# Kernel optimization log

Measured on AMD Instinct MI355X. Metric: run time of the kernel, lower is better.

## Reference

```python
import jax, jax.numpy as jnp
import numpy as np
from jax import lax

B, T, F, C = 2, 249, 64, 256   # fixed by alpha/beta weight shapes in build()
K = 3                          # conv kernel size
FILT = 256                     # q/k conv filters (both blocks)
V = 256                        # v conv filters (both blocks)
OUT_CH = 64                    # conv2d_final filters (hardcoded)


def conv2d(x, w, b):
    # NHWC 'same' conv, stride 1, dilation 1
    return lax.conv_general_dilated(
        x, w, window_strides=(1, 1), padding='SAME',
        dimension_numbers=('NHWC', 'HWIO', 'NHWC')) + b


def attn_block(x, wq, bq, wk, bk, wv, bv):
    # x: [B, H, L, C]; attention over L per (batch, H) slice
    q = conv2d(x, wq, bq)          # [B,H,L,FILT]
    k = conv2d(x, wk, bk)          # [B,H,L,FILT]
    v = conv2d(x, wv, bv)          # [B,H,L,V]
    scores = jnp.einsum('bhqc,bhkc->bhqk', q, k)   # [B,H,L,L]
    dist = jax.nn.softmax(scores, axis=-1)
    return jnp.einsum('bhqk,bhkc->bhqc', dist, v)  # [B,H,L,V]


def setup_inputs() -> dict:
    key = jax.random.key(0)
    ks = jax.random.split(key, 18)
    s = 0.05
    d = {'x': jax.random.normal(ks[0], (B, T, F, C), jnp.float32)}
    names = ['wq_f', 'wk_f', 'wv_f', 'wq_t', 'wk_t', 'wv_t']
    outs = [FILT, FILT, V, FILT, FILT, V]
    for i, (n, o) in enumerate(zip(names, outs)):
        d[n] = jax.random.normal(ks[1 + i], (K, K, C, o), jnp.float32) * s
        d['b' + n[1:]] = jnp.zeros((o,), jnp.float32)
    d['w_final'] = jax.random.normal(ks[8], (K, K, V + V + C, OUT_CH), jnp.float32) * s
    d['b_final'] = jnp.zeros((OUT_CH,), jnp.float32)
    d['alpha'] = jax.random.uniform(ks[9], (B, T, F, V), jnp.float32, -0.05, 0.05)
    d['beta'] = jax.random.uniform(ks[10], (B, T, F, V), jnp.float32, -0.05, 0.05)
    return d


def reference(x, wq_f, bq_f, wk_f, bk_f, wv_f, bv_f,
              wq_t, bq_t, wk_t, bk_t, wv_t, bv_t,
              w_final, b_final, alpha, beta):
    # AFAB: transpose to [B,F,T,C], attend over time axis T
    xt = jnp.transpose(x, (0, 2, 1, 3))
    out_freq = attn_block(xt, wq_f, bq_f, wk_f, bk_f, wv_f, bv_f)
    out_freq = jnp.transpose(out_freq, (0, 2, 1, 3))  # back to [B,T,F,V]
    # ATAB: attend over frequency axis F directly on [B,T,F,C]
    out_time = attn_block(x, wq_t, bq_t, wk_t, bk_t, wv_t, bv_t)
    # learned elementwise gating + concat + final conv (concatenation=True path)
    fused = jnp.concatenate([alpha * out_freq, beta * out_time, x], axis=-1)
    return conv2d(fused, w_final, b_final)
```

## Files before the change

### kernel.cpp

```cpp
#include <hip/hip_runtime.h>


typedef _Float16 f16;
typedef _Float16 f16x8 __attribute__((ext_vector_type(8)));
typedef float    f32x4 __attribute__((ext_vector_type(4)));

#define B_   2
#define T_   249
#define F_   64
#define TP   251
#define FP   66
#define PIXB (T_*F_)
#define NPIX (B_*PIXB)
#define LPAD 256
#define XPOS (B_*TP*FP)

static constexpr size_t FUSED_BYTES = (size_t)B_*TP*FP*768*2;
static constexpr size_t XPAD_BYTES  = (size_t)B_*TP*FP*256*2;
static constexpr size_t QF_BYTES    = (size_t)B_*64*LPAD*256*2;
static constexpr size_t QT_BYTES    = (size_t)B_*T_*64*256*2;
static constexpr size_t WT_BYTES    = (size_t)9*1536*256*2;
static constexpr size_t WFT_BYTES   = (size_t)9*64*768*2;

static constexpr size_t OFF_FUSED = 0;
static constexpr size_t OFF_XPAD  = OFF_FUSED + FUSED_BYTES;
static constexpr size_t OFF_QF    = OFF_XPAD  + XPAD_BYTES;
static constexpr size_t OFF_KF    = OFF_QF + QF_BYTES;
static constexpr size_t OFF_VF    = OFF_KF + QF_BYTES;
static constexpr size_t OFF_QT    = OFF_VF + QF_BYTES;
static constexpr size_t OFF_KT    = OFF_QT + QT_BYTES;
static constexpr size_t OFF_VT    = OFF_KT + QT_BYTES;
static constexpr size_t OFF_WT    = OFF_VT + QT_BYTES;
static constexpr size_t OFF_WFT   = OFF_WT + WT_BYTES;
static constexpr size_t OFF_BALL  = OFF_WFT + WFT_BYTES;
static constexpr size_t OFF_BF    = OFF_BALL + 1536*4;
static constexpr size_t WS_NEED   = OFF_BF + 64*4;

__device__ __forceinline__ f32x4 mfma16(f16x8 a, f16x8 b, f32x4 c) {
    return __builtin_amdgcn_mfma_f32_16x16x32_f16(a, b, c, 0, 0, 0);
}

__device__ __forceinline__ void gl_lds16(const void* g, void* l) {
    __builtin_amdgcn_global_load_lds(
        (const __attribute__((address_space(1))) unsigned int*)(unsigned long long)g,
        (__attribute__((address_space(3))) unsigned int*)(unsigned int)(unsigned long long)l,
        16, 0, 0);
}

__global__ __launch_bounds__(256) void prep_w(
    const float* __restrict__ wqf, const float* __restrict__ wkf, const float* __restrict__ wvf,
    const float* __restrict__ wqt, const float* __restrict__ wkt, const float* __restrict__ wvt,
    const float* __restrict__ wfin,
    const float* __restrict__ bqf, const float* __restrict__ bkf, const float* __restrict__ bvf,
    const float* __restrict__ bqt, const float* __restrict__ bkt, const float* __restrict__ bvt,
    const float* __restrict__ bfin,
    f16* __restrict__ wT, f16* __restrict__ wfT,
    float* __restrict__ biasAll, float* __restrict__ biasF)
{
    int idx = blockIdx.x*256 + threadIdx.x;
    if (idx < 9*1536*256) {
        int tap = idx / (1536*256);
        int r   = idx - tap*(1536*256);
        int n = r >> 8, c = r & 255;
        int dt = tap/3 - 1, df = tap%3 - 1;
        int blk = n >> 8, nl = n & 255;
        const float* w; int kh, kw;
        if (blk < 3) { w = (blk==0) ? wqf : (blk==1) ? wkf : wvf; kh = df+1; kw = dt+1; }
        else         { w = (blk==3) ? wqt : (blk==4) ? wkt : wvt; kh = dt+1; kw = df+1; }
        wT[idx] = (f16)w[((kh*3 + kw)*256 + c)*256 + nl];
    }
    if (idx < 9*64*768) {
        int tap = idx / (64*768);
        int r   = idx - tap*(64*768);
        int oc = r / 768, cin = r - oc*768;
        int dt = tap/3 - 1, df = tap%3 - 1;
        wfT[idx] = (f16)wfin[(((dt+1)*3 + (df+1))*768 + cin)*64 + oc];
    }
    if (idx < 1536) {
        int blk = idx >> 8, nl = idx & 255;
        const float* bb = (blk==0)?bqf:(blk==1)?bkf:(blk==2)?bvf:(blk==3)?bqt:(blk==4)?bkt:bvt;
        biasAll[idx] = bb[nl];
    }
    if (idx < 64) biasF[idx] = bfin[idx];
}

__global__ __launch_bounds__(256) void prep_x(
    const float* __restrict__ x, f16* __restrict__ xpad, f16* __restrict__ fused)
{
    int tid = blockIdx.x*256 + threadIdx.x;
    int pix = tid >> 5, c8 = (tid & 31)*8;
    int b = pix / PIXB; int r = pix - b*PIXB;
    int t = r >> 6, f = r & 63;
    const float* src = x + (size_t)pix*256 + c8;
    f16x8 v;
#pragma unroll
    for (int j = 0; j < 8; ++j) v[j] = (f16)src[j];
    size_t pp = (size_t)(b*TP + t + 1)*FP + (f + 1);
    *(f16x8*)(xpad + pp*256 + c8) = v;
    *(f16x8*)(fused + pp*768 + 512 + c8) = v;
}

__global__ __launch_bounds__(256) void border_zero(
    f16* __restrict__ xpad, f16* __restrict__ fused)
{
    int pix = blockIdx.x*2 + (threadIdx.x >> 7);
    int tl = threadIdx.x & 127;
    int b = pix / 630; int i = pix - b*630;
    int tp, fp;
    if (i < 66)       { tp = 0;   fp = i; }
    else if (i < 132) { tp = 250; fp = i - 66; }
    else { int j = i - 132; tp = 1 + (j >> 1); fp = (j & 1) * 65; }
    size_t pp = (size_t)(b*TP + tp)*FP + fp;
    f16x8 z = {0, 0, 0, 0, 0, 0, 0, 0};
    if (tl < 32) *(f16x8*)(xpad + pp*256 + tl*8) = z;
    if (tl < 96) *(f16x8*)(fused + pp*768 + tl*8) = z;
}

__global__ __launch_bounds__(512, 2) void conv_qkv(
    const f16* __restrict__ xpad, const f16* __restrict__ wT,
    const float* __restrict__ biasAll,
    f16* __restrict__ qf, f16* __restrict__ kf, f16* __restrict__ vf,
    f16* __restrict__ qt, f16* __restrict__ kt_, f16* __restrict__ vt)
{
    __shared__ f16 smemH[448*64];
    __shared__ f16 smemB[2][256*64];

    const int xcd = blockIdx.x & 7, lin = blockIdx.x >> 3;
    const int mtcnt = (xcd < 6) ? 16 : 15;
    if (lin >= 6*mtcnt) return;
    const int mtbase = (xcd < 6) ? xcd*16 : 96 + (xcd - 6)*15;
    const int nt = lin / mtcnt;
    const int mt = mtbase + (lin - nt*mtcnt);

    const int bb_ = mt / 63;
    const int t0  = (mt - bb_*63) * 4;
    const int Gs66 = (bb_*TP + t0) * 66;

    const int l   = threadIdx.x & 63;
    const int wid = threadIdx.x >> 6;
    const int wm = wid >> 2, wn = wid & 3;

    int hOff[7];
#pragma unroll
    for (int j = 0; j < 7; ++j) {
        int pos = j*64 + wid*8 + (l >> 3);
        int ps = pos;
        if (ps > 395) ps = 395;
        { int pm = XPOS - 1 - (bb_*TP + t0)*66; if (ps > pm) ps = pm; }
        int ch = (l & 7) ^ (ps & 7);
        hOff[j] = (Gs66 + ps)*256 + ch*8;
    }
    int bSrc[4];
#pragma unroll
    for (int j = 0; j < 4; ++j) {
        int row = j*64 + wid*8 + (l >> 3);
        int ch = (l & 7) ^ (row & 7);
        bSrc[j] = (nt*256 + row)*256 + ch*8;
    }

    int pos00[8];
#pragma unroll
    for (int m = 0; m < 8; ++m) {
        int r = wm*128 + m*16 + (l & 15);
        pos00[m] = ((r >> 6) + 1)*66 + (r & 63) + 1;
    }
    int bRow[4], bSw[4];
#pragma unroll
    for (int n = 0; n < 4; ++n) {
        int row = wn*64 + n*16 + (l & 15);
        bRow[n] = row*64; bSw[n] = row & 7;
    }

    f32x4 acc[8][4];
#pragma unroll
    for (int m = 0; m < 8; ++m)
#pragma unroll
        for (int n = 0; n < 4; ++n) acc[m][n] = {0.f, 0.f, 0.f, 0.f};

#define HSTAGE(C) do {                                                         \
        _Pragma("unroll")                                                      \
        for (int j_ = 0; j_ < 7; ++j_)                                         \
            gl_lds16(xpad + hOff[j_] + (C)*64,                                 \
                     smemH + (j_*512 + wid*64)*8);                             \
    } while (0)

#define BSTAGE(TAP, C, NB) do {                                                \
        const f16* wt_ = wT + (size_t)(TAP)*(1536*256) + (C)*64;               \
        _Pragma("unroll")                                                      \
        for (int j_ = 0; j_ < 4; ++j_)                                         \
            gl_lds16(wt_ + bSrc[j_], &smemB[NB][(j_*512 + wid*64)*8]);         \
    } while (0)

#define QCOMP(NB, TAPOFF) do {                                                 \
        int pos_[8];                                                           \
        _Pragma("unroll")                                                      \
        for (int m = 0; m < 8; ++m) pos_[m] = pos00[m] + (TAPOFF);             \
        _Pragma("unroll")                                                      \
        for (int kk = 0; kk < 2; ++kk) {                                       \
            const int cch = kk*4 + (l >> 4);                                   \
            f16x8 af[8], bf[4];                                                \
            _Pragma("unroll")                                                  \
            for (int m = 0; m < 8; ++m)                                        \
                af[m] = *(const f16x8*)(smemH + pos_[m]*64 + ((cch ^ (pos_[m] & 7)) << 3)); \
            _Pragma("unroll")                                                  \
            for (int n = 0; n < 4; ++n)                                        \
                bf[n] = *(const f16x8*)(&smemB[NB][0] + bRow[n] + ((cch ^ bSw[n]) << 3)); \
            __builtin_amdgcn_s_setprio(1);                                     \
            _Pragma("unroll")                                                  \
            for (int m = 0; m < 8; ++m)                                        \
                _Pragma("unroll")                                              \
                for (int n = 0; n < 4; ++n)                                    \
                    acc[m][n] = mfma16(af[m], bf[n], acc[m][n]);               \
            __builtin_amdgcn_s_setprio(0);                                     \
        }                                                                      \
    } while (0)

    int buf = 0;
    HSTAGE(0);
    BSTAGE(0, 0, 0);
    __syncthreads();
    for (int c = 0; c < 4; ++c) {
        for (int tap = 0; tap < 9; ++tap) {
            if (tap < 8)      BSTAGE(tap + 1, c, buf ^ 1);
            else if (c < 3)   BSTAGE(0, c + 1, buf ^ 1);
            const int dt = tap/3 - 1, df = tap - (tap/3)*3 - 1;
            QCOMP(buf, dt*66 + df);
            __syncthreads();
            buf ^= 1;
        }
        if (c < 3) {
            HSTAGE(c + 1);
            __syncthreads();
        }
    }
#undef HSTAGE
#undef BSTAGE
#undef QCOMP

    f16* dst = (nt==0)?qf:(nt==1)?kf:(nt==2)?vf:(nt==3)?qt:(nt==4)?kt_:vt;
#pragma unroll
    for (int m = 0; m < 8; ++m) {
#pragma unroll
        for (int rg = 0; rg < 4; ++rg) {
            int row = wm*128 + m*16 + (l >> 4)*4 + rg;
            int t = t0 + (row >> 6), f = row & 63;
            if (t <= 248) {
#pragma unroll
                for (int n = 0; n < 4; ++n) {
                    int col = wn*64 + n*16 + (l & 15);
                    float v = acc[m][n][rg] + biasAll[nt*256 + col];
                    int off;
                    if (nt < 2)       off = ((bb_*64 + f)*LPAD + t)*256 + col;
                    else if (nt == 2) off = ((bb_*64 + f)*256 + col)*LPAD + t;
                    else if (nt < 5)  off = ((bb_*T_ + t)*64 + f)*256 + col;
                    else              off = ((bb_*T_ + t)*256 + col)*64 + f;
                    dst[off] = (f16)v;
                }
            }
        }
    }
}

__global__ __launch_bounds__(256) void attn_f(
    const f16* __restrict__ qf, const f16* __restrict__ kf, const f16* __restrict__ vf,
    const float* __restrict__ alpha, f16* __restrict__ fused)
{
    __shared__ f16 plds[4][16*256];
    const int l = threadIdx.x & 63;
    const int wid = threadIdx.x >> 6;
    const int head = blockIdx.x >> 2;
    const int qb = blockIdx.x & 3;
    const int b = head >> 6, f = head & 63;
    const f16* qh = qf + (size_t)head*LPAD*256;
    const f16* kh = kf + (size_t)head*LPAD*256;
    const f16* vh = vf + (size_t)head*256*LPAD;
    const int qr0 = qb*64 + wid*16;
    f16* pw = &plds[wid][0];

    f16x8 qa[8];
#pragma unroll
    for (int ks = 0; ks < 8; ++ks)
        qa[ks] = *(const f16x8*)(qh + (qr0 + (l & 15))*256 + ks*32 + (l >> 4)*8);

    f32x4 s[16];
#pragma unroll
    for (int nf = 0; nf < 16; ++nf) s[nf] = {0.f, 0.f, 0.f, 0.f};
#pragma unroll
    for (int ks = 0; ks < 8; ++ks)
#pragma unroll
        for (int nf = 0; nf < 16; ++nf) {
            f16x8 bf = *(const f16x8*)(kh + (nf*16 + (l & 15))*256 + ks*32 + (l >> 4)*8);
            s[nf] = mfma16(qa[ks], bf, s[nf]);
        }

    float inv[4];
#pragma unroll
    for (int rg = 0; rg < 4; ++rg) {
        float m = -1e30f;
#pragma unroll
        for (int nf = 0; nf < 16; ++nf)
            if (nf*16 + (l & 15) < T_) m = fmaxf(m, s[nf][rg]);
#pragma unroll
        for (int d = 1; d < 16; d <<= 1) m = fmaxf(m, __shfl_xor(m, d, 64));
        float sum = 0.f;
#pragma unroll
        for (int nf = 0; nf < 16; ++nf) {
            float p = (nf*16 + (l & 15) < T_) ? __expf(s[nf][rg] - m) : 0.f;
            s[nf][rg] = p;
            sum += p;
        }
#pragma unroll
        for (int d = 1; d < 16; d <<= 1) sum += __shfl_xor(sum, d, 64);
        inv[rg] = 1.f / sum;
    }

#pragma unroll
    for (int nf = 0; nf < 16; ++nf)
#pragma unroll
        for (int rg = 0; rg < 4; ++rg) {
            int row = (l >> 4)*4 + rg;
            int col = nf*16 + (l & 15);
            int byte = (row*512 + col*2) ^ ((row & 7) << 4);
            *(f16*)((char*)pw + byte) = (f16)s[nf][rg];
        }

    f32x4 o[16];
#pragma unroll
    for (int nf = 0; nf < 16; ++nf) o[nf] = {0.f, 0.f, 0.f, 0.f};
#pragma unroll
    for (int ks = 0; ks < 8; ++ks) {
        int row = l & 15;
        int cch = ks*4 + (l >> 4);
        int byte = row*512 + ((cch ^ (row & 7)) << 4);
        f16x8 pa = *(const f16x8*)((const char*)pw + byte);
#pragma unroll
        for (int nf = 0; nf < 16; ++nf) {
            f16x8 bf = *(const f16x8*)(vh + (nf*16 + (l & 15))*LPAD + ks*32 + (l >> 4)*8);
            o[nf] = mfma16(pa, bf, o[nf]);
        }
    }

#pragma unroll
    for (int rg = 0; rg < 4; ++rg) {
        int t = qr0 + (l >> 4)*4 + rg;
        if (t < T_) {
#pragma unroll
            for (int nf = 0; nf < 16; ++nf) {
                int c = nf*16 + (l & 15);
                float v = o[nf][rg] * inv[rg] * alpha[((size_t)(b*T_ + t)*64 + f)*256 + c];
                fused[((size_t)(b*TP + t + 1)*FP + (f + 1))*768 + c] = (f16)v;
            }
        }
    }
}

__global__ __launch_bounds__(256) void attn_t(
    const f16* __restrict__ qt, const f16* __restrict__ kt, const f16* __restrict__ vt,
    const float* __restrict__ beta, f16* __restrict__ fused)
{
    __shared__ f16 plds[4][16*64];
    const int l = threadIdx.x & 63;
    const int wid = threadIdx.x >> 6;
    const int head = blockIdx.x;
    const int b = head / T_, t = head - b*T_;
    const f16* qh = qt + (size_t)head*64*256;
    const f16* kh = kt + (size_t)head*64*256;
    const f16* vh = vt + (size_t)head*256*64;
    const int qr0 = wid*16;
    f16* pw = &plds[wid][0];

    f16x8 qa[8];
#pragma unroll
    for (int ks = 0; ks < 8; ++ks)
        qa[ks] = *(const f16x8*)(qh + (qr0 + (l & 15))*256 + ks*32 + (l >> 4)*8);

    f32x4 s[4];
#pragma unroll
    for (int nf = 0; nf < 4; ++nf) s[nf] = {0.f, 0.f, 0.f, 0.f};
#pragma unroll
    for (int ks = 0; ks < 8; ++ks)
#pragma unroll
        for (int nf = 0; nf < 4; ++nf) {
            f16x8 bf = *(const f16x8*)(kh + (nf*16 + (l & 15))*256 + ks*32 + (l >> 4)*8);
            s[nf] = mfma16(qa[ks], bf, s[nf]);
        }

    float inv[4];
#pragma unroll
    for (int rg = 0; rg < 4; ++rg) {
        float m = -1e30f;
#pragma unroll
        for (int nf = 0; nf < 4; ++nf) m = fmaxf(m, s[nf][rg]);
#pragma unroll
        for (int d = 1; d < 16; d <<= 1) m = fmaxf(m, __shfl_xor(m, d, 64));
        float sum = 0.f;
#pragma unroll
        for (int nf = 0; nf < 4; ++nf) {
            float p = __expf(s[nf][rg] - m);
            s[nf][rg] = p;
            sum += p;
        }
#pragma unroll
        for (int d = 1; d < 16; d <<= 1) sum += __shfl_xor(sum, d, 64);
        inv[rg] = 1.f / sum;
    }

#pragma unroll
    for (int nf = 0; nf < 4; ++nf)
#pragma unroll
        for (int rg = 0; rg < 4; ++rg) {
            int row = (l >> 4)*4 + rg;
            int col = nf*16 + (l & 15);
            int byte = (row*128 + col*2) ^ ((row & 7) << 4);
            *(f16*)((char*)pw + byte) = (f16)s[nf][rg];
        }

    f32x4 o[16];
#pragma unroll
    for (int nf = 0; nf < 16; ++nf) o[nf] = {0.f, 0.f, 0.f, 0.f};
#pragma unroll
    for (int ks = 0; ks < 2; ++ks) {
        int row = l & 15;
        int cch = ks*4 + (l >> 4);
        int byte = row*128 + ((cch ^ (row & 7)) << 4);
        f16x8 pa = *(const f16x8*)((const char*)pw + byte);
#pragma unroll
        for (int nf = 0; nf < 16; ++nf) {
            f16x8 bf = *(const f16x8*)(vh + (nf*16 + (l & 15))*64 + ks*32 + (l >> 4)*8);
            o[nf] = mfma16(pa, bf, o[nf]);
        }
    }

#pragma unroll
    for (int rg = 0; rg < 4; ++rg) {
        int fo = qr0 + (l >> 4)*4 + rg;
#pragma unroll
        for (int nf = 0; nf < 16; ++nf) {
            int c = nf*16 + (l & 15);
            float v = o[nf][rg] * inv[rg] * beta[((size_t)(b*T_ + t)*64 + fo)*256 + c];
            fused[((size_t)(b*TP + t + 1)*FP + (fo + 1))*768 + 256 + c] = (f16)v;
        }
    }
}

__global__ __launch_bounds__(256, 2) void conv_final(
    const f16* __restrict__ fused, const f16* __restrict__ wfT,
    const float* __restrict__ biasF, float* __restrict__ out)
{
    __shared__ f16 smemH[288*64];
    __shared__ f16 smemB[2][64*64];

    const int mt = blockIdx.x;
    const int bb = mt / 125;
    const int t0 = (mt - bb*125) * 2;
    const int Gs66 = (bb*TP + t0) * 66;

    const int tid = threadIdx.x;
    const int l   = tid & 63;
    const int wid = tid >> 6;
    const int wm = wid >> 1, wn = wid & 1;

    int hOff[9];
#pragma unroll
    for (int j = 0; j < 9; ++j) {
        int ps = j*32 + (tid >> 3);
        if (ps > 263) ps = 263;
        { int pm = XPOS - 1 - (bb*TP + t0)*66; if (ps > pm) ps = pm; }
        int ch = (tid & 7) ^ (ps & 7);
        hOff[j] = (Gs66 + ps)*768 + ch*8;
    }
    int bSrc[2];
#pragma unroll
    for (int j = 0; j < 2; ++j) {
        int row = j*32 + (tid >> 3);
        int ch  = (tid & 7) ^ (row & 7);
        bSrc[j] = row*768 + ch*8;
    }

    int pos00[4];
#pragma unroll
    for (int m = 0; m < 4; ++m) {
        int r = wm*64 + m*16 + (l & 15);
        pos00[m] = ((r >> 6) + 1)*66 + (r & 63) + 1;
    }
    int bRow[2], bSw[2];
#pragma unroll
    for (int n = 0; n < 2; ++n) {
        int row = wn*32 + n*16 + (l & 15);
        bRow[n] = row*64; bSw[n] = row & 7;
    }

    f32x4 acc[4][2];
#pragma unroll
    for (int m = 0; m < 4; ++m)
#pragma unroll
        for (int n = 0; n < 2; ++n) acc[m][n] = {0.f, 0.f, 0.f, 0.f};

#define FHSTAGE(C) do {                                                        \
        _Pragma("unroll")                                                      \
        for (int j_ = 0; j_ < 9; ++j_)                                         \
            gl_lds16(fused + hOff[j_] + (C)*64,                                \
                     smemH + (j_*256 + wid*64)*8);                             \
    } while (0)

#define FBSTAGE(TAP, C, NB) do {                                               \
        const f16* wt_ = wfT + (size_t)(TAP)*(64*768) + (C)*64;                \
        _Pragma("unroll")                                                      \
        for (int j_ = 0; j_ < 2; ++j_)                                         \
            gl_lds16(wt_ + bSrc[j_], &smemB[NB][(j_*256 + wid*64)*8]);         \
    } while (0)

#define FCOMP(NB, TAPOFF) do {                                                 \
        int pos_[4];                                                           \
        _Pragma("unroll")                                                      \
        for (int m = 0; m < 4; ++m) pos_[m] = pos00[m] + (TAPOFF);             \
        _Pragma("unroll")                                                      \
        for (int kk = 0; kk < 2; ++kk) {                                       \
            const int cch = kk*4 + (l >> 4);                                   \
            f16x8 af[4], bf[2];                                                \
            _Pragma("unroll")                                                  \
            for (int m = 0; m < 4; ++m)                                        \
                af[m] = *(const f16x8*)(smemH + pos_[m]*64 + ((cch ^ (pos_[m] & 7)) << 3)); \
            _Pragma("unroll")                                                  \
            for (int n = 0; n < 2; ++n)                                        \
                bf[n] = *(const f16x8*)(&smemB[NB][0] + bRow[n] + ((cch ^ bSw[n]) << 3)); \
            __builtin_amdgcn_s_setprio(1);                                     \
            _Pragma("unroll")                                                  \
            for (int m = 0; m < 4; ++m)                                        \
                _Pragma("unroll")                                              \
                for (int n = 0; n < 2; ++n)                                    \
                    acc[m][n] = mfma16(af[m], bf[n], acc[m][n]);               \
            __builtin_amdgcn_s_setprio(0);                                     \
        }                                                                      \
    } while (0)

    int buf = 0;
    FHSTAGE(0);
    FBSTAGE(0, 0, 0);
    __syncthreads();
    for (int c = 0; c < 12; ++c) {
        for (int tap = 0; tap < 9; ++tap) {
            if (tap < 8)       FBSTAGE(tap + 1, c, buf ^ 1);
            else if (c < 11)   FBSTAGE(0, c + 1, buf ^ 1);
            const int dt = tap/3 - 1, df = tap - (tap/3)*3 - 1;
            FCOMP(buf, dt*66 + df);
            __syncthreads();
            buf ^= 1;
        }
        if (c < 11) {
            FHSTAGE(c + 1);
            __syncthreads();
        }
    }
#undef FHSTAGE
#undef FBSTAGE
#undef FCOMP

#pragma unroll
    for (int m = 0; m < 4; ++m) {
#pragma unroll
        for (int rg = 0; rg < 4; ++rg) {
            int r = wm*64 + m*16 + (l >> 4)*4 + rg;
            int t = t0 + (r >> 6), f = r & 63;
            if (t <= 248) {
                size_t pix = (size_t)bb*PIXB + t*64 + f;
#pragma unroll
                for (int n = 0; n < 2; ++n) {
                    int oc = wn*32 + n*16 + (l & 15);
                    out[pix*64 + oc] = acc[m][n][rg] + biasF[oc];
                }
            }
        }
    }
}

extern "C" void kernel_launch(void* const* d_in, const int* in_sizes, int n_in,
                              void* d_out, int out_size, void* d_ws, size_t ws_size,
                              hipStream_t stream) {
    (void)in_sizes; (void)n_in; (void)out_size;
    const float* x    = (const float*)d_in[0];
    const float* wqf  = (const float*)d_in[1];
    const float* bqf  = (const float*)d_in[2];
    const float* wkf  = (const float*)d_in[3];
    const float* bkf  = (const float*)d_in[4];
    const float* wvf  = (const float*)d_in[5];
    const float* bvf  = (const float*)d_in[6];
    const float* wqt  = (const float*)d_in[7];
    const float* bqt  = (const float*)d_in[8];
    const float* wkt  = (const float*)d_in[9];
    const float* bkt  = (const float*)d_in[10];
    const float* wvt  = (const float*)d_in[11];
    const float* bvt  = (const float*)d_in[12];
    const float* wfin = (const float*)d_in[13];
    const float* bfin = (const float*)d_in[14];
    const float* alpha= (const float*)d_in[15];
    const float* beta = (const float*)d_in[16];

    if (ws_size < WS_NEED) return;

    char* ws = (char*)d_ws;
    f16* fused  = (f16*)(ws + OFF_FUSED);
    f16* xpad   = (f16*)(ws + OFF_XPAD);
    f16* qf     = (f16*)(ws + OFF_QF);
    f16* kf     = (f16*)(ws + OFF_KF);
    f16* vf     = (f16*)(ws + OFF_VF);
    f16* qt     = (f16*)(ws + OFF_QT);
    f16* kt     = (f16*)(ws + OFF_KT);
    f16* vt     = (f16*)(ws + OFF_VT);
    f16* wT     = (f16*)(ws + OFF_WT);
    f16* wfT    = (f16*)(ws + OFF_WFT);
    float* bAll = (float*)(ws + OFF_BALL);
    float* bF   = (float*)(ws + OFF_BF);

    hipMemsetAsync(vf, 0, QF_BYTES, stream);

    border_zero<<<dim3(630), dim3(256), 0, stream>>>(xpad, fused);
    prep_w<<<dim3((9*1536*256 + 255)/256), dim3(256), 0, stream>>>(
        wqf, wkf, wvf, wqt, wkt, wvt, wfin,
        bqf, bkf, bvf, bqt, bkt, bvt, bfin, wT, wfT, bAll, bF);
    prep_x<<<dim3(NPIX*32/256), dim3(256), 0, stream>>>(x, xpad, fused);
    conv_qkv<<<dim3(768), dim3(512), 0, stream>>>(xpad, wT, bAll, qf, kf, vf, qt, kt, vt);
    attn_f<<<dim3(512), dim3(256), 0, stream>>>(qf, kf, vf, alpha, fused);
    attn_t<<<dim3(498), dim3(256), 0, stream>>>(qt, kt, vt, beta, fused);
    conv_final<<<dim3(250), dim3(256), 0, stream>>>(fused, wfT, bF, (float*)d_out);
}
```

Baseline: 502.2 us.

## Restructure qkv conv pipeline, transpose weights via LDS, replace vf memset

The qkv convolution drops the halo-staged input tile with a per-tap weight double buffer. It now uses a 36-step K loop that double-buffers both the A (shifted input pixels) and B (weights) 32-channel chunks through global_load_lds, with explicit waitcnt, barriers and sched barriers to overlap loads with MFMA. Weight prep becomes an LDS-tiled transpose kernel for coalesced reads plus a separate kernel for the final-conv weights and biases. The full memset of vf is replaced by a small kernel that zeroes only the padded time columns. The new conv reloads A per tap instead of reusing a halo tile, and drops the occupancy hint of 2 blocks, which could raise input traffic or lower occupancy.

```diff
diff --git a/kernel.cpp b/kernel.cpp
--- a/kernel.cpp
+++ b/kernel.cpp
@@ -47,28 +47,44 @@
         16, 0, 0);
 }
 
-__global__ __launch_bounds__(256) void prep_w(
+__global__ __launch_bounds__(256) void prep_wT(
     const float* __restrict__ wqf, const float* __restrict__ wkf, const float* __restrict__ wvf,
     const float* __restrict__ wqt, const float* __restrict__ wkt, const float* __restrict__ wvt,
+    f16* __restrict__ wT)
+{
+    __shared__ float lt[64][257];
+    const int bid = blockIdx.x;
+    const int tap = bid / 24;
+    const int rr  = bid - tap*24;
+    const int blk = rr >> 2, cq = rr & 3;
+    const int dt = tap/3 - 1, df = tap%3 - 1;
+    const float* w; int kh, kw;
+    if (blk < 3) { w = (blk==0) ? wqf : (blk==1) ? wkf : wvf; kh = df+1; kw = dt+1; }
+    else         { w = (blk==3) ? wqt : (blk==4) ? wkt : wvt; kh = dt+1; kw = df+1; }
+    const int c0 = cq*64;
+    const int tid = threadIdx.x;
+
+    const float* src = w + ((size_t)(kh*3 + kw)*256 + c0)*256 + tid;
+    for (int cr = 0; cr < 64; ++cr)
+        lt[cr][tid] = src[(size_t)cr*256];
+    __syncthreads();
+
+    const int cc = tid & 63, ng = tid >> 6;
+    f16* dst = wT + ((size_t)tap*1536 + blk*256)*256 + c0 + cc;
+    for (int j = 0; j < 64; ++j) {
+        int n = j*4 + ng;
+        dst[(size_t)n*256] = (f16)lt[cc][n];
+    }
+}
+
+__global__ __launch_bounds__(256) void prep_wmisc(
     const float* __restrict__ wfin,
     const float* __restrict__ bqf, const float* __restrict__ bkf, const float* __restrict__ bvf,
     const float* __restrict__ bqt, const float* __restrict__ bkt, const float* __restrict__ bvt,
     const float* __restrict__ bfin,
-    f16* __restrict__ wT, f16* __restrict__ wfT,
-    float* __restrict__ biasAll, float* __restrict__ biasF)
+    f16* __restrict__ wfT, float* __restrict__ biasAll, float* __restrict__ biasF)
 {
     int idx = blockIdx.x*256 + threadIdx.x;
-    if (idx < 9*1536*256) {
-        int tap = idx / (1536*256);
-        int r   = idx - tap*(1536*256);
-        int n = r >> 8, c = r & 255;
-        int dt = tap/3 - 1, df = tap%3 - 1;
-        int blk = n >> 8, nl = n & 255;
-        const float* w; int kh, kw;
-        if (blk < 3) { w = (blk==0) ? wqf : (blk==1) ? wkf : wvf; kh = df+1; kw = dt+1; }
-        else         { w = (blk==3) ? wqt : (blk==4) ? wkt : wvt; kh = dt+1; kw = df+1; }
-        wT[idx] = (f16)w[((kh*3 + kw)*256 + c)*256 + nl];
-    }
     if (idx < 9*64*768) {
         int tap = idx / (64*768);
         int r   = idx - tap*(64*768);
@@ -116,14 +132,23 @@
     if (tl < 96) *(f16x8*)(fused + pp*768 + tl*8) = z;
 }
 
-__global__ __launch_bounds__(512, 2) void conv_qkv(
+__global__ __launch_bounds__(256) void vf_pad(f16* __restrict__ vf)
+{
+    int head = blockIdx.x;
+    int c = threadIdx.x;
+    f16* p = vf + ((size_t)head*256 + c)*LPAD;
+#pragma unroll
+    for (int t = T_; t < LPAD; ++t) p[t] = (f16)0.f;
+}
+
+__global__ __launch_bounds__(512) void conv_qkv(
     const f16* __restrict__ xpad, const f16* __restrict__ wT,
     const float* __restrict__ biasAll,
     f16* __restrict__ qf, f16* __restrict__ kf, f16* __restrict__ vf,
     f16* __restrict__ qt, f16* __restrict__ kt_, f16* __restrict__ vt)
 {
-    __shared__ f16 smemH[448*64];
-    __shared__ f16 smemB[2][256*64];
+    __shared__ f16 smemA[2*2*8192];
+    __shared__ f16 smemB[2*2*8192];
 
     const int xcd = blockIdx.x & 7, lin = blockIdx.x >> 3;
     const int mtcnt = (xcd < 6) ? 16 : 15;
@@ -132,43 +157,38 @@
     const int nt = lin / mtcnt;
     const int mt = mtbase + (lin - nt*mtcnt);
 
-    const int bb_ = mt / 63;
-    const int t0  = (mt - bb_*63) * 4;
-    const int Gs66 = (bb_*TP + t0) * 66;
-
-    const int l   = threadIdx.x & 63;
-    const int wid = threadIdx.x >> 6;
+    const int bb = mt / 63;
+    const int tloc = mt - bb*63;
+
+    const int tid = threadIdx.x;
+    const int l   = tid & 63;
+    const int wid = tid >> 6;
     const int wm = wid >> 2, wn = wid & 3;
-
-    int hOff[7];
-#pragma unroll
-    for (int j = 0; j < 7; ++j) {
-        int pos = j*64 + wid*8 + (l >> 3);
-        int ps = pos;
-        if (ps > 395) ps = 395;
-        { int pm = XPOS - 1 - (bb_*TP + t0)*66; if (ps > pm) ps = pm; }
-        int ch = (l & 7) ^ (ps & 7);
-        hOff[j] = (Gs66 + ps)*256 + ch*8;
-    }
-    int bSrc[4];
-#pragma unroll
-    for (int j = 0; j < 4; ++j) {
-        int row = j*64 + wid*8 + (l >> 3);
-        int ch = (l & 7) ^ (row & 7);
-        bSrc[j] = (nt*256 + row)*256 + ch*8;
-    }
-
-    int pos00[8];
+    const int g  = l >> 4;
+
+    int aS[2], bS[2];
+#pragma unroll
+    for (int u = 0; u < 2; ++u) {
+        int idx = u*512 + tid;
+        int r = idx >> 2, oct = idx & 3;
+        int go = oct ^ (r & 3);
+        int pib = tloc*256 + r; if (pib > PIXB-1) pib = PIXB-1;
+        int t = pib >> 6, f = pib & 63;
+        aS[u] = ((bb*TP + t + 1)*FP + (f + 1))*256 + go*8;
+        bS[u] = (nt*256 + r)*256 + go*8;
+    }
+
+    int lrA[8], kA[8];
 #pragma unroll
     for (int m = 0; m < 8; ++m) {
-        int r = wm*128 + m*16 + (l & 15);
-        pos00[m] = ((r >> 6) + 1)*66 + (r & 63) + 1;
-    }
-    int bRow[4], bSw[4];
+        int lr = wm*128 + m*16 + (l & 15);
+        lrA[m] = lr*32; kA[m] = lr & 3;
+    }
+    int lrB[4], kB[4];
 #pragma unroll
     for (int n = 0; n < 4; ++n) {
-        int row = wn*64 + n*16 + (l & 15);
-        bRow[n] = row*64; bSw[n] = row & 7;
+        int lr = wn*64 + n*16 + (l & 15);
+        lrB[n] = lr*32; kB[n] = lr & 3;
     }
 
     f32x4 acc[8][4];
@@ -177,65 +197,104 @@
 #pragma unroll
         for (int n = 0; n < 4; ++n) acc[m][n] = {0.f, 0.f, 0.f, 0.f};
 
-#define HSTAGE(C) do {                                                         \
+#define SB   __builtin_amdgcn_sched_barrier(0)
+#define BARR __builtin_amdgcn_s_barrier()
+#define LGKM asm volatile("s_waitcnt lgkmcnt(0)" ::: "memory")
+#define VM4  asm volatile("s_waitcnt vmcnt(4)" ::: "memory")
+#define VM0  asm volatile("s_waitcnt vmcnt(0)" ::: "memory")
+#define RDA(S, BASE) do {                                                      \
         _Pragma("unroll")                                                      \
-        for (int j_ = 0; j_ < 7; ++j_)                                         \
-            gl_lds16(xpad + hOff[j_] + (C)*64,                                 \
-                     smemH + (j_*512 + wid*64)*8);                             \
+        for (int m_ = 0; m_ < 4; ++m_)                                         \
+            af[m_] = *(const f16x8*)((BASE) + lrA[(S)*4 + m_]                  \
+                                     + ((g ^ kA[(S)*4 + m_]) << 3));           \
     } while (0)
-
-#define BSTAGE(TAP, C, NB) do {                                                \
-        const f16* wt_ = wT + (size_t)(TAP)*(1536*256) + (C)*64;               \
+#define RDB(BASE) do {                                                         \
         _Pragma("unroll")                                                      \
-        for (int j_ = 0; j_ < 4; ++j_)                                         \
-            gl_lds16(wt_ + bSrc[j_], &smemB[NB][(j_*512 + wid*64)*8]);         \
+        for (int n_ = 0; n_ < 4; ++n_)                                         \
+            bf[n_] = *(const f16x8*)((BASE) + lrB[n_]                          \
+                                     + ((g ^ kB[n_]) << 3));                   \
     } while (0)
-
-#define QCOMP(NB, TAPOFF) do {                                                 \
-        int pos_[8];                                                           \
+#define MM(S) do {                                                             \
+        __builtin_amdgcn_s_setprio(1);                                         \
         _Pragma("unroll")                                                      \
-        for (int m = 0; m < 8; ++m) pos_[m] = pos00[m] + (TAPOFF);             \
-        _Pragma("unroll")                                                      \
-        for (int kk = 0; kk < 2; ++kk) {                                       \
-            const int cch = kk*4 + (l >> 4);                                   \
-            f16x8 af[8], bf[4];                                                \
+        for (int m_ = 0; m_ < 4; ++m_)                                         \
             _Pragma("unroll")                                                  \
-            for (int m = 0; m < 8; ++m)                                        \
-                af[m] = *(const f16x8*)(smemH + pos_[m]*64 + ((cch ^ (pos_[m] & 7)) << 3)); \
-            _Pragma("unroll")                                                  \
-            for (int n = 0; n < 4; ++n)                                        \
-                bf[n] = *(const f16x8*)(&smemB[NB][0] + bRow[n] + ((cch ^ bSw[n]) << 3)); \
-            __builtin_amdgcn_s_setprio(1);                                     \
-            _Pragma("unroll")                                                  \
-            for (int m = 0; m < 8; ++m)                                        \
-                _Pragma("unroll")                                              \
-                for (int n = 0; n < 4; ++n)                                    \
-                    acc[m][n] = mfma16(af[m], bf[n], acc[m][n]);               \
-            __builtin_amdgcn_s_setprio(0);                                     \
-        }                                                                      \
+            for (int n_ = 0; n_ < 4; ++n_)                                     \
+                acc[(S)*4 + m_][n_] = mfma16(af[m_], bf[n_], acc[(S)*4 + m_][n_]); \
+        __builtin_amdgcn_s_setprio(0);                                         \
     } while (0)
-
-    int buf = 0;
-    HSTAGE(0);
-    BSTAGE(0, 0, 0);
-    __syncthreads();
-    for (int c = 0; c < 4; ++c) {
-        for (int tap = 0; tap < 9; ++tap) {
-            if (tap < 8)      BSTAGE(tap + 1, c, buf ^ 1);
-            else if (c < 3)   BSTAGE(0, c + 1, buf ^ 1);
-            const int dt = tap/3 - 1, df = tap - (tap/3)*3 - 1;
-            QCOMP(buf, dt*66 + df);
-            __syncthreads();
-            buf ^= 1;
-        }
-        if (c < 3) {
-            HSTAGE(c + 1);
-            __syncthreads();
-        }
-    }
-#undef HSTAGE
-#undef BSTAGE
-#undef QCOMP
+#define GA(DST, U, HOFF) \
+        gl_lds16(xpad + aS[U] + ashn + (HOFF), (DST) + ((U)*512 + wid*64)*8)
+#define GB(DST, U, HOFF) \
+        gl_lds16(wT + bS[U] + bshn + (HOFF), (DST) + ((U)*512 + wid*64)*8)
+
+    {
+        const int ashn = (-1*FP - 1)*256;
+        const size_t bshn = 0;
+        GA(smemA + 0*8192, 0, 0);  GA(smemA + 0*8192, 1, 0);
+        GB(smemB + 0*8192, 0, 0);  GB(smemB + 0*8192, 1, 0);
+        GA(smemA + 1*8192, 0, 32); GA(smemA + 1*8192, 1, 32);
+        GB(smemB + 1*8192, 0, 32); GB(smemB + 1*8192, 1, 32);
+        SB; VM4; BARR; SB;
+    }
+
+#pragma unroll 1
+    for (int kt = 0; kt < 36; ++kt) {
+        const int db = kt & 1;
+        const f16* Ac0 = smemA + (db*2 + 0)*8192;
+        const f16* Ac1 = smemA + (db*2 + 1)*8192;
+        const f16* Bc0 = smemB + (db*2 + 0)*8192;
+        const f16* Bc1 = smemB + (db*2 + 1)*8192;
+        f16* An0 = smemA + ((db^1)*2 + 0)*8192;
+        f16* An1 = smemA + ((db^1)*2 + 1)*8192;
+        f16* Bn0 = smemB + ((db^1)*2 + 0)*8192;
+        f16* Bn1 = smemB + ((db^1)*2 + 1)*8192;
+        const int ktn = kt + 1;
+        const bool st = ktn < 36;
+        const int tapn = ktn >> 2, kcn = ktn & 3;
+        const int ashn = st ? ((tapn/3 - 1)*FP + (tapn%3 - 1))*256 + kcn*64 : 0;
+        const size_t bshn = st ? (size_t)tapn*(1536*256) + kcn*64 : 0;
+
+        f16x8 af[4], bf[4];
+
+        RDB(Bc0); RDA(0, Ac0);
+        if (st) { GA(An0, 0, 0); GA(An0, 1, 0); }
+        SB; BARR; LGKM; SB;
+        MM(0);
+        SB; BARR;
+
+        RDA(1, Ac0);
+        if (st) { GB(Bn0, 0, 0); GB(Bn0, 1, 0); }
+        SB; BARR; LGKM; SB;
+        MM(1);
+        SB;
+        if (kt < 35) VM4; else VM0;
+        BARR;
+
+        RDB(Bc1); RDA(0, Ac1);
+        if (st) { GA(An1, 0, 32); GA(An1, 1, 32); }
+        SB; BARR; LGKM; SB;
+        MM(0);
+        SB; BARR;
+
+        RDA(1, Ac1);
+        if (st) { GB(Bn1, 0, 32); GB(Bn1, 1, 32); }
+        SB; BARR; LGKM; SB;
+        MM(1);
+        SB;
+        if (kt < 35) VM4; else VM0;
+        BARR;
+    }
+#undef SB
+#undef BARR
+#undef LGKM
+#undef VM4
+#undef VM0
+#undef RDA
+#undef RDB
+#undef MM
+#undef GA
+#undef GB
 
     f16* dst = (nt==0)?qf:(nt==1)?kf:(nt==2)?vf:(nt==3)?qt:(nt==4)?kt_:vt;
 #pragma unroll
@@ -243,17 +302,18 @@
 #pragma unroll
         for (int rg = 0; rg < 4; ++rg) {
             int row = wm*128 + m*16 + (l >> 4)*4 + rg;
-            int t = t0 + (row >> 6), f = row & 63;
+            int pib = tloc*256 + row;
+            int t = pib >> 6, f = pib & 63;
             if (t <= 248) {
 #pragma unroll
                 for (int n = 0; n < 4; ++n) {
                     int col = wn*64 + n*16 + (l & 15);
                     float v = acc[m][n][rg] + biasAll[nt*256 + col];
                     int off;
-                    if (nt < 2)       off = ((bb_*64 + f)*LPAD + t)*256 + col;
-                    else if (nt == 2) off = ((bb_*64 + f)*256 + col)*LPAD + t;
-                    else if (nt < 5)  off = ((bb_*T_ + t)*64 + f)*256 + col;
-                    else              off = ((bb_*T_ + t)*256 + col)*64 + f;
+                    if (nt < 2)       off = ((bb*64 + f)*LPAD + t)*256 + col;
+                    else if (nt == 2) off = ((bb*64 + f)*256 + col)*LPAD + t;
+                    else if (nt < 5)  off = ((bb*T_ + t)*64 + f)*256 + col;
+                    else              off = ((bb*T_ + t)*256 + col)*64 + f;
                     dst[off] = (f16)v;
                 }
             }
@@ -612,12 +672,11 @@
     float* bAll = (float*)(ws + OFF_BALL);
     float* bF   = (float*)(ws + OFF_BF);
 
-    hipMemsetAsync(vf, 0, QF_BYTES, stream);
-
     border_zero<<<dim3(630), dim3(256), 0, stream>>>(xpad, fused);
-    prep_w<<<dim3((9*1536*256 + 255)/256), dim3(256), 0, stream>>>(
-        wqf, wkf, wvf, wqt, wkt, wvt, wfin,
-        bqf, bkf, bvf, bqt, bkt, bvt, bfin, wT, wfT, bAll, bF);
+    vf_pad<<<dim3(128), dim3(256), 0, stream>>>(vf);
+    prep_wT<<<dim3(216), dim3(256), 0, stream>>>(wqf, wkf, wvf, wqt, wkt, wvt, wT);
+    prep_wmisc<<<dim3(1728), dim3(256), 0, stream>>>(
+        wfin, bqf, bkf, bvf, bqt, bkt, bvt, bfin, wfT, bAll, bF);
     prep_x<<<dim3(NPIX*32/256), dim3(256), 0, stream>>>(x, xpad, fused);
     conv_qkv<<<dim3(768), dim3(512), 0, stream>>>(xpad, wT, bAll, qf, kf, vf, qt, kt, vt);
     attn_f<<<dim3(512), dim3(256), 0, stream>>>(qf, kf, vf, alpha, fused);
```

Result: slower. 514.9 us (+2.5%).
